# Kernel optimization log

Hardware: AMD Instinct MI355X
Metric: run time of the kernel (lower is better)

The kernel has to match this reference:

```python
import jax, jax.numpy as jnp
import numpy as np

# Vanilla tanh-RNN (num_layers=1, batch_first) followed by tanh + dropout(eval: identity) + linear.

def setup_inputs() -> dict:
    key = jax.random.key(0)
    ks = jax.random.split(key, 7)
    B, T, I, H, C = 16384, 64, 64, 100, 40
    s_ih = 1.0 / np.sqrt(H)
    return {
        "x": jax.random.normal(ks[0], (B, T * I), dtype=jnp.float32),
        "W_ih": jax.random.normal(ks[1], (H, I), dtype=jnp.float32) * s_ih,
        "W_hh": jax.random.normal(ks[2], (H, H), dtype=jnp.float32) * s_ih,
        "b_ih": jax.random.normal(ks[3], (H,), dtype=jnp.float32) * s_ih,
        "b_hh": jax.random.normal(ks[4], (H,), dtype=jnp.float32) * s_ih,
        "fc_W": jax.random.normal(ks[5], (C, H), dtype=jnp.float32) * 0.1,
        "fc_b": jax.random.normal(ks[6], (C,), dtype=jnp.float32) * 0.1,
    }


def reference(x, W_ih, W_hh, b_ih, b_hh, fc_W, fc_b):
    B = x.shape[0]
    x = x.reshape(B, 64, 64)  # [B, T, I]
    # Precompute input projections for all steps in one GEMM: [B, T, H]
    xp = jnp.einsum("bti,hi->bth", x, W_ih) + b_ih + b_hh
    h0 = jnp.zeros((B, W_hh.shape[0]), dtype=x.dtype)

    def step(h, xp_t):  # h: [B, H], xp_t: [B, H]
        h_new = jnp.tanh(xp_t + h @ W_hh.T)
        return h_new, None

    h_last, _ = jax.lax.scan(step, h0, jnp.swapaxes(xp, 0, 1))  # scan over T
    out = jnp.tanh(h_last)  # tanh on last-step output
    # dropout(p=0.2) in eval mode = identity
    return out @ fc_W.T + fc_b  # [B, 40]
```

## Files before the change

### kernel.cpp

```cpp
#include <hip/hip_runtime.h>


typedef _Float16 half8 __attribute__((ext_vector_type(8)));
typedef float float4_t __attribute__((ext_vector_type(4)));

__device__ __forceinline__ float tanh_fast(float x) {
  float e = __builtin_amdgcn_exp2f(x * 2.8853900817779268f);
  return 1.0f - 2.0f * __builtin_amdgcn_rcpf(e + 1.0f);
}

__global__ __launch_bounds__(256, 1) void rnn_fused(
    const float* __restrict__ x, const float* __restrict__ W_ih,
    const float* __restrict__ W_hh, const float* __restrict__ b_ih,
    const float* __restrict__ b_hh, const float* __restrict__ fc_W,
    const float* __restrict__ fc_b, float* __restrict__ out, int B)
{
  const int lane = threadIdx.x & 63;
  const int wave = threadIdx.x >> 6;
  const int g = lane >> 4;
  const int c = lane & 15;
  const int rowbase = (blockIdx.x * 4 + wave) * 16;

  half8 wih[2][7];
  half8 whh[4][7];
  float4_t bias[7];

  #pragma unroll
  for (int nt = 0; nt < 7; ++nt) {
    int nb = nt * 16 + 4 * g;
    float4_t bi = {0.f, 0.f, 0.f, 0.f};
    if (nb + 3 < 100) {
      float4_t a = *(const float4_t*)(b_ih + nb);
      float4_t b = *(const float4_t*)(b_hh + nb);
      bi = a + b;
    }
    bias[nt] = bi;

    int nrow = nt * 16 + c;
    bool rv = (nrow < 100);
    #pragma unroll
    for (int kb = 0; kb < 2; ++kb) {
      float4_t f0 = {0.f,0.f,0.f,0.f}, f1 = {0.f,0.f,0.f,0.f};
      if (rv) {
        const float* p = W_ih + nrow * 64 + kb * 32 + g * 8;
        f0 = *(const float4_t*)p;
        f1 = *(const float4_t*)(p + 4);
      }
      half8 h;
      #pragma unroll
      for (int j = 0; j < 4; ++j) { h[j] = (_Float16)f0[j]; h[4 + j] = (_Float16)f1[j]; }
      wih[kb][nt] = h;
    }
    #pragma unroll
    for (int kb = 0; kb < 4; ++kb) {
      int clo = kb * 32 + 4 * g;
      int chi = clo + 16;
      float4_t f0 = {0.f,0.f,0.f,0.f}, f1 = {0.f,0.f,0.f,0.f};
      if (rv && clo + 3 < 100) f0 = *(const float4_t*)(W_hh + nrow * 100 + clo);
      if (rv && chi + 3 < 100) f1 = *(const float4_t*)(W_hh + nrow * 100 + chi);
      half8 h;
      #pragma unroll
      for (int j = 0; j < 4; ++j) { h[j] = (_Float16)f0[j]; h[4 + j] = (_Float16)f1[j]; }
      whh[kb][nt] = h;
    }
  }

  const float* xrow = x + (size_t)(rowbase + c) * 4096 + g * 8;
  float4_t s0, s1, s2, s3;
  float4_t p0, p1, p2, p3;
  {
    const float* p = xrow;
    s0 = *(const float4_t*)p;        s1 = *(const float4_t*)(p + 4);
    s2 = *(const float4_t*)(p + 32); s3 = *(const float4_t*)(p + 36);
    p += 64;
    p0 = *(const float4_t*)p;        p1 = *(const float4_t*)(p + 4);
    p2 = *(const float4_t*)(p + 32); p3 = *(const float4_t*)(p + 36);
  }

  float4_t acc[7];
  half8 hfrag[4];
  #pragma unroll
  for (int kb = 0; kb < 4; ++kb) hfrag[kb] = (half8)(_Float16)0.0f;

  for (int t = 0; t < 64; ++t) {
    float4_t q0 = {0.f,0.f,0.f,0.f}, q1 = q0, q2 = q0, q3 = q0;
    if (t < 62) {
      const float* p = xrow + (t + 2) * 64;
      q0 = *(const float4_t*)p;        q1 = *(const float4_t*)(p + 4);
      q2 = *(const float4_t*)(p + 32); q3 = *(const float4_t*)(p + 36);
    }

    half8 xb0, xb1;
    #pragma unroll
    for (int j = 0; j < 4; ++j) {
      xb0[j] = (_Float16)s0[j]; xb0[4 + j] = (_Float16)s1[j];
      xb1[j] = (_Float16)s2[j]; xb1[4 + j] = (_Float16)s3[j];
    }

    #pragma unroll
    for (int nt = 0; nt < 7; ++nt) {
      acc[nt] = __builtin_amdgcn_mfma_f32_16x16x32_f16(wih[0][nt], xb0, bias[nt], 0, 0, 0);
      acc[nt] = __builtin_amdgcn_mfma_f32_16x16x32_f16(wih[1][nt], xb1, acc[nt], 0, 0, 0);
    }
    #pragma unroll
    for (int kb = 0; kb < 4; ++kb)
      #pragma unroll
      for (int nt = 0; nt < 7; ++nt)
        acc[nt] = __builtin_amdgcn_mfma_f32_16x16x32_f16(whh[kb][nt], hfrag[kb], acc[nt], 0, 0, 0);

    #pragma unroll
    for (int nt = 0; nt < 7; ++nt)
      #pragma unroll
      for (int v = 0; v < 4; ++v)
        acc[nt][v] = tanh_fast(acc[nt][v]);

    #pragma unroll
    for (int kb = 0; kb < 4; ++kb) {
      half8 h;
      #pragma unroll
      for (int v = 0; v < 4; ++v) {
        h[v] = (_Float16)acc[2 * kb][v];
        h[4 + v] = (kb < 3) ? (_Float16)acc[2 * kb + 1][v] : (_Float16)0.0f;
      }
      hfrag[kb] = h;
    }

    s0 = p0; s1 = p1; s2 = p2; s3 = p3;
    p0 = q0; p1 = q1; p2 = q2; p3 = q3;
  }

  #pragma unroll
  for (int nt = 0; nt < 7; ++nt)
    #pragma unroll
    for (int v = 0; v < 4; ++v)
      acc[nt][v] = tanh_fast(acc[nt][v]);
  #pragma unroll
  for (int kb = 0; kb < 4; ++kb) {
    half8 h;
    #pragma unroll
    for (int v = 0; v < 4; ++v) {
      h[v] = (_Float16)acc[2 * kb][v];
      h[4 + v] = (kb < 3) ? (_Float16)acc[2 * kb + 1][v] : (_Float16)0.0f;
    }
    hfrag[kb] = h;
  }

  half8 wfc[4][3];
  float4_t bfc[3];
  #pragma unroll
  for (int nt = 0; nt < 3; ++nt) {
    int nb = nt * 16 + 4 * g;
    float4_t bi = {0.f,0.f,0.f,0.f};
    if (nb + 3 < 40) bi = *(const float4_t*)(fc_b + nb);
    bfc[nt] = bi;

    int nrow = nt * 16 + c;
    bool rv = (nrow < 40);
    #pragma unroll
    for (int kb = 0; kb < 4; ++kb) {
      int clo = kb * 32 + 4 * g;
      int chi = clo + 16;
      float4_t f0 = {0.f,0.f,0.f,0.f}, f1 = {0.f,0.f,0.f,0.f};
      if (rv && clo + 3 < 100) f0 = *(const float4_t*)(fc_W + nrow * 100 + clo);
      if (rv && chi + 3 < 100) f1 = *(const float4_t*)(fc_W + nrow * 100 + chi);
      half8 h;
      #pragma unroll
      for (int j = 0; j < 4; ++j) { h[j] = (_Float16)f0[j]; h[4 + j] = (_Float16)f1[j]; }
      wfc[kb][nt] = h;
    }
  }

  float4_t oacc[3];
  #pragma unroll
  for (int nt = 0; nt < 3; ++nt) oacc[nt] = bfc[nt];
  #pragma unroll
  for (int kb = 0; kb < 4; ++kb)
    #pragma unroll
    for (int nt = 0; nt < 3; ++nt)
      oacc[nt] = __builtin_amdgcn_mfma_f32_16x16x32_f16(wfc[kb][nt], hfrag[kb], oacc[nt], 0, 0, 0);

  #pragma unroll
  for (int nt = 0; nt < 3; ++nt)
    #pragma unroll
    for (int v = 0; v < 4; ++v) {
      int n = nt * 16 + 4 * g + v;
      if (n < 40)
        out[(size_t)(rowbase + c) * 40 + n] = oacc[nt][v];
    }
}

extern "C" void kernel_launch(void* const* d_in, const int* in_sizes, int n_in,
                              void* d_out, int out_size, void* d_ws, size_t ws_size,
                              hipStream_t stream) {
  const float* x    = (const float*)d_in[0];
  const float* W_ih = (const float*)d_in[1];
  const float* W_hh = (const float*)d_in[2];
  const float* b_ih = (const float*)d_in[3];
  const float* b_hh = (const float*)d_in[4];
  const float* fc_W = (const float*)d_in[5];
  const float* fc_b = (const float*)d_in[6];
  float* outp = (float*)d_out;

  int B = in_sizes[0] / 4096;
  int grid = (B + 63) / 64;
  rnn_fused<<<grid, 256, 0, stream>>>(x, W_ih, W_hh, b_ih, b_hh, fc_W, fc_b, outp, B);
}
```

Before: 68.48 us.

## Stream x tiles into per-wave LDS ring via async global_load_lds

Replaces per-lane strided register prefetch of x with a 4-slot per-wave LDS ring filled by global_load_lds, three timesteps ahead, using coalesced row chunks with a padded layout (17-float stride). Also reorders the MFMAs so the recurrent W_hh products come first, giving the LDS reads time to land before the input-projection MFMAs. This aims at better-coalesced global loads and less register pressure, at the cost of LDS traffic and a hand-written vmcnt wait that relies on the exact count of outstanding loads.

```diff
diff --git a/kernel.cpp b/kernel.cpp
--- a/kernel.cpp
+++ b/kernel.cpp
@@ -3,6 +3,12 @@
 
 typedef _Float16 half8 __attribute__((ext_vector_type(8)));
 typedef float float4_t __attribute__((ext_vector_type(4)));
+
+#define SLOT_BYTES 5120
+#define GLOAD16(gp, lp)                                                   \
+  __builtin_amdgcn_global_load_lds(                                       \
+      (const __attribute__((address_space(1))) void*)(gp),                \
+      (__attribute__((address_space(3))) void*)(lp), 16, 0, 0)
 
 __device__ __forceinline__ float tanh_fast(float x) {
   float e = __builtin_amdgcn_exp2f(x * 2.8853900817779268f);
@@ -15,11 +21,13 @@
     const float* __restrict__ b_hh, const float* __restrict__ fc_W,
     const float* __restrict__ fc_b, float* __restrict__ out, int B)
 {
+  __shared__ char ring[4][4 * SLOT_BYTES];
   const int lane = threadIdx.x & 63;
   const int wave = threadIdx.x >> 6;
   const int g = lane >> 4;
   const int c = lane & 15;
   const int rowbase = (blockIdx.x * 4 + wave) * 16;
+  char* ring_w = &ring[wave][0];
 
   half8 wih[2][7];
   half8 whh[4][7];
@@ -65,30 +73,54 @@
     }
   }
 
-  const float* xrow = x + (size_t)(rowbase + c) * 4096 + g * 8;
-  float4_t s0, s1, s2, s3;
-  float4_t p0, p1, p2, p3;
-  {
-    const float* p = xrow;
-    s0 = *(const float4_t*)p;        s1 = *(const float4_t*)(p + 4);
-    s2 = *(const float4_t*)(p + 32); s3 = *(const float4_t*)(p + 36);
-    p += 64;
-    p0 = *(const float4_t*)p;        p1 = *(const float4_t*)(p + 4);
-    p2 = *(const float4_t*)(p + 32); p3 = *(const float4_t*)(p + 36);
-  }
+  const float* gsrc[5];
+  #pragma unroll
+  for (int j = 0; j < 5; ++j) {
+    int m = j * 64 + lane;
+    int r = (m * 3856) >> 16;
+    int c17 = m - r * 17;
+    bool valid = (r < 16) & (c17 < 16);
+    int row = rowbase + (valid ? r : 0);
+    int col = valid ? c17 * 4 : 0;
+    gsrc[j] = x + (size_t)row * 4096 + col;
+  }
+
+  #pragma unroll
+  for (int s = 0; s < 3; ++s)
+    #pragma unroll
+    for (int j = 0; j < 5; ++j)
+      GLOAD16(gsrc[j] + s * 64, ring_w + s * SLOT_BYTES + j * 1024);
 
   float4_t acc[7];
   half8 hfrag[4];
   #pragma unroll
   for (int kb = 0; kb < 4; ++kb) hfrag[kb] = (half8)(_Float16)0.0f;
 
+  const int roff = c * 272 + g * 32;
+
   for (int t = 0; t < 64; ++t) {
-    float4_t q0 = {0.f,0.f,0.f,0.f}, q1 = q0, q2 = q0, q3 = q0;
-    if (t < 62) {
-      const float* p = xrow + (t + 2) * 64;
-      q0 = *(const float4_t*)p;        q1 = *(const float4_t*)(p + 4);
-      q2 = *(const float4_t*)(p + 32); q3 = *(const float4_t*)(p + 36);
-    }
+    int tp = t + 3; if (tp > 63) tp = 63;
+    char* lb = ring_w + ((t + 3) & 3) * SLOT_BYTES;
+    #pragma unroll
+    for (int j = 0; j < 5; ++j)
+      GLOAD16(gsrc[j] + tp * 64, lb + j * 1024);
+
+    asm volatile("s_waitcnt vmcnt(15)" ::: "memory");
+
+    const char* sp = ring_w + (t & 3) * SLOT_BYTES + roff;
+    float4_t s0 = *(const float4_t*)(sp);
+    float4_t s1 = *(const float4_t*)(sp + 16);
+    float4_t s2 = *(const float4_t*)(sp + 128);
+    float4_t s3 = *(const float4_t*)(sp + 144);
+
+    #pragma unroll
+    for (int nt = 0; nt < 7; ++nt)
+      acc[nt] = __builtin_amdgcn_mfma_f32_16x16x32_f16(whh[0][nt], hfrag[0], bias[nt], 0, 0, 0);
+    #pragma unroll
+    for (int kb = 1; kb < 4; ++kb)
+      #pragma unroll
+      for (int nt = 0; nt < 7; ++nt)
+        acc[nt] = __builtin_amdgcn_mfma_f32_16x16x32_f16(whh[kb][nt], hfrag[kb], acc[nt], 0, 0, 0);
 
     half8 xb0, xb1;
     #pragma unroll
@@ -96,17 +128,11 @@
       xb0[j] = (_Float16)s0[j]; xb0[4 + j] = (_Float16)s1[j];
       xb1[j] = (_Float16)s2[j]; xb1[4 + j] = (_Float16)s3[j];
     }
-
     #pragma unroll
     for (int nt = 0; nt < 7; ++nt) {
-      acc[nt] = __builtin_amdgcn_mfma_f32_16x16x32_f16(wih[0][nt], xb0, bias[nt], 0, 0, 0);
+      acc[nt] = __builtin_amdgcn_mfma_f32_16x16x32_f16(wih[0][nt], xb0, acc[nt], 0, 0, 0);
       acc[nt] = __builtin_amdgcn_mfma_f32_16x16x32_f16(wih[1][nt], xb1, acc[nt], 0, 0, 0);
     }
-    #pragma unroll
-    for (int kb = 0; kb < 4; ++kb)
-      #pragma unroll
-      for (int nt = 0; nt < 7; ++nt)
-        acc[nt] = __builtin_amdgcn_mfma_f32_16x16x32_f16(whh[kb][nt], hfrag[kb], acc[nt], 0, 0, 0);
 
     #pragma unroll
     for (int nt = 0; nt < 7; ++nt)
@@ -124,9 +150,6 @@
       }
       hfrag[kb] = h;
     }
-
-    s0 = p0; s1 = p1; s2 = p2; s3 = p3;
-    p0 = q0; p1 = q1; p2 = q2; p3 = q3;
   }
 
   #pragma unroll
```

Result: faster. 65.51 us (-4.3%).

## Split hidden-state tiles across two waves with LDS exchange and async x prefetch ring

Applied to the files above, without the earlier changes.

Each 16-row batch tile is now processed by two waves that split the 7 hidden output tiles (4 and 3). The waves exchange their halves of the hidden state through a double-buffered LDS area, with a barrier every step. The x input is streamed into a 4-slot LDS ring using global_load_lds direct loads issued three steps ahead, replacing per-thread register prefetch. This halves the per-wave MFMA chain on the recurrent critical path and quadruples the block count, at the cost of a per-step barrier and LDS round trip.

```diff
diff --git a/kernel.cpp b/kernel.cpp
--- a/kernel.cpp
+++ b/kernel.cpp
@@ -3,30 +3,44 @@
 
 typedef _Float16 half8 __attribute__((ext_vector_type(8)));
 typedef float float4_t __attribute__((ext_vector_type(4)));
+
+#define SLOT_BYTES 6144
+#define RING_BYTES (4 * SLOT_BYTES)
+#define HX_BYTES 4096
+#define GLOAD16(gp, lp)                                                   \
+  __builtin_amdgcn_global_load_lds(                                       \
+      (const __attribute__((address_space(1))) void*)(gp),                \
+      (__attribute__((address_space(3))) void*)(lp), 16, 0, 0)
 
 __device__ __forceinline__ float tanh_fast(float x) {
   float e = __builtin_amdgcn_exp2f(x * 2.8853900817779268f);
   return 1.0f - 2.0f * __builtin_amdgcn_rcpf(e + 1.0f);
 }
 
-__global__ __launch_bounds__(256, 1) void rnn_fused(
+template <int NTBASE, int NTN, int FCB, int FCN>
+__device__ __forceinline__ void run_tile(
     const float* __restrict__ x, const float* __restrict__ W_ih,
     const float* __restrict__ W_hh, const float* __restrict__ b_ih,
     const float* __restrict__ b_hh, const float* __restrict__ fc_W,
-    const float* __restrict__ fc_b, float* __restrict__ out, int B)
+    const float* __restrict__ fc_b, float* __restrict__ out,
+    int rowbase, int lane, int wave, char* ldsp)
 {
-  const int lane = threadIdx.x & 63;
-  const int wave = threadIdx.x >> 6;
   const int g = lane >> 4;
   const int c = lane & 15;
-  const int rowbase = (blockIdx.x * 4 + wave) * 16;
-
-  half8 wih[2][7];
-  half8 whh[4][7];
-  float4_t bias[7];
-
-  #pragma unroll
-  for (int nt = 0; nt < 7; ++nt) {
+  constexpr int K0 = NTBASE / 2;
+  constexpr int FKB = K0 ^ 2;
+
+  const unsigned ring_base =
+      (unsigned)(uintptr_t)(__attribute__((address_space(3))) char*)ldsp;
+  const unsigned hx_base = ring_base + RING_BYTES;
+
+  half8 wih[2][NTN];
+  half8 whh[4][NTN];
+  float4_t bias[NTN];
+
+  #pragma unroll
+  for (int nl = 0; nl < NTN; ++nl) {
+    int nt = NTBASE + nl;
     int nb = nt * 16 + 4 * g;
     float4_t bi = {0.f, 0.f, 0.f, 0.f};
     if (nb + 3 < 100) {
@@ -34,7 +48,7 @@
       float4_t b = *(const float4_t*)(b_hh + nb);
       bi = a + b;
     }
-    bias[nt] = bi;
+    bias[nl] = bi;
 
     int nrow = nt * 16 + c;
     bool rv = (nrow < 100);
@@ -49,7 +63,7 @@
       half8 h;
       #pragma unroll
       for (int j = 0; j < 4; ++j) { h[j] = (_Float16)f0[j]; h[4 + j] = (_Float16)f1[j]; }
-      wih[kb][nt] = h;
+      wih[kb][nl] = h;
     }
     #pragma unroll
     for (int kb = 0; kb < 4; ++kb) {
@@ -61,33 +75,74 @@
       half8 h;
       #pragma unroll
       for (int j = 0; j < 4; ++j) { h[j] = (_Float16)f0[j]; h[4 + j] = (_Float16)f1[j]; }
-      whh[kb][nt] = h;
-    }
-  }
-
-  const float* xrow = x + (size_t)(rowbase + c) * 4096 + g * 8;
-  float4_t s0, s1, s2, s3;
-  float4_t p0, p1, p2, p3;
+      whh[kb][nl] = h;
+    }
+  }
+
+  const float* gsrc[3];
+  #pragma unroll
+  for (int j = 0; j < 3; ++j) {
+    int m = j * 128 + wave * 64 + lane;
+    int r = (m * 3856) >> 16;
+    int c17 = m - r * 17;
+    bool valid = (r < 16) & (c17 < 16);
+    int row = rowbase + (valid ? r : 0);
+    int col = valid ? c17 * 4 : 0;
+    gsrc[j] = x + (size_t)row * 4096 + col;
+  }
+
+  #pragma unroll
+  for (int s = 0; s < 3; ++s) {
+    char* lb = ldsp + s * SLOT_BYTES + wave * 1024;
+    GLOAD16(gsrc[0] + s * 64, lb);
+    GLOAD16(gsrc[1] + s * 64, lb + 2048);
+    GLOAD16(gsrc[2] + s * 64, lb + 4096);
+  }
+
+  half8 own0 = (half8)(_Float16)0.0f;
+  half8 own1 = (half8)(_Float16)0.0f;
   {
-    const float* p = xrow;
-    s0 = *(const float4_t*)p;        s1 = *(const float4_t*)(p + 4);
-    s2 = *(const float4_t*)(p + 32); s3 = *(const float4_t*)(p + 36);
-    p += 64;
-    p0 = *(const float4_t*)p;        p1 = *(const float4_t*)(p + 4);
-    p2 = *(const float4_t*)(p + 32); p3 = *(const float4_t*)(p + 36);
-  }
-
-  float4_t acc[7];
-  half8 hfrag[4];
-  #pragma unroll
-  for (int kb = 0; kb < 4; ++kb) hfrag[kb] = (half8)(_Float16)0.0f;
+    unsigned wa = hx_base + K0 * 1024 + c * 64 + g * 16;
+    asm volatile(
+        "ds_write_b128 %0, %1 offset:0\n\t"
+        "ds_write_b128 %0, %2 offset:1024"
+        :: "v"(wa), "v"(__builtin_bit_cast(float4_t, own0)),
+           "v"(__builtin_bit_cast(float4_t, own1)));
+  }
+  asm volatile("s_waitcnt vmcnt(6) lgkmcnt(0)\n\ts_barrier" ::: "memory");
+
+  float4_t acc[4];
 
   for (int t = 0; t < 64; ++t) {
-    float4_t q0 = {0.f,0.f,0.f,0.f}, q1 = q0, q2 = q0, q3 = q0;
-    if (t < 62) {
-      const float* p = xrow + (t + 2) * 64;
-      q0 = *(const float4_t*)p;        q1 = *(const float4_t*)(p + 4);
-      q2 = *(const float4_t*)(p + 32); q3 = *(const float4_t*)(p + 36);
+    unsigned ha = hx_base + (t & 1) * HX_BYTES + FKB * 1024 + c * 64 + g * 16;
+    unsigned xa = ring_base + (t & 3) * SLOT_BYTES + c * 272 + g * 32;
+    float4_t fh0, fh1, s0, s1, s2, s3;
+    asm volatile(
+        "ds_read_b128 %0, %6 offset:0\n\t"
+        "ds_read_b128 %1, %6 offset:1024\n\t"
+        "ds_read_b128 %2, %7 offset:0\n\t"
+        "ds_read_b128 %3, %7 offset:16\n\t"
+        "ds_read_b128 %4, %7 offset:128\n\t"
+        "ds_read_b128 %5, %7 offset:144"
+        : "=&v"(fh0), "=&v"(fh1), "=&v"(s0), "=&v"(s1), "=&v"(s2), "=&v"(s3)
+        : "v"(ha), "v"(xa));
+
+    #pragma unroll
+    for (int nl = 0; nl < NTN; ++nl) {
+      acc[nl] = __builtin_amdgcn_mfma_f32_16x16x32_f16(whh[K0][nl], own0, bias[nl], 0, 0, 0);
+      acc[nl] = __builtin_amdgcn_mfma_f32_16x16x32_f16(whh[K0 + 1][nl], own1, acc[nl], 0, 0, 0);
+    }
+
+    asm volatile("s_waitcnt lgkmcnt(0)"
+                 : "+v"(fh0), "+v"(fh1), "+v"(s0), "+v"(s1), "+v"(s2), "+v"(s3));
+    __builtin_amdgcn_sched_barrier(0);
+
+    half8 fr0 = __builtin_bit_cast(half8, fh0);
+    half8 fr1 = __builtin_bit_cast(half8, fh1);
+    #pragma unroll
+    for (int nl = 0; nl < NTN; ++nl) {
+      acc[nl] = __builtin_amdgcn_mfma_f32_16x16x32_f16(whh[FKB][nl], fr0, acc[nl], 0, 0, 0);
+      acc[nl] = __builtin_amdgcn_mfma_f32_16x16x32_f16(whh[FKB + 1][nl], fr1, acc[nl], 0, 0, 0);
     }
 
     half8 xb0, xb1;
@@ -96,65 +151,89 @@
       xb0[j] = (_Float16)s0[j]; xb0[4 + j] = (_Float16)s1[j];
       xb1[j] = (_Float16)s2[j]; xb1[4 + j] = (_Float16)s3[j];
     }
-
-    #pragma unroll
-    for (int nt = 0; nt < 7; ++nt) {
-      acc[nt] = __builtin_amdgcn_mfma_f32_16x16x32_f16(wih[0][nt], xb0, bias[nt], 0, 0, 0);
-      acc[nt] = __builtin_amdgcn_mfma_f32_16x16x32_f16(wih[1][nt], xb1, acc[nt], 0, 0, 0);
-    }
-    #pragma unroll
-    for (int kb = 0; kb < 4; ++kb)
-      #pragma unroll
-      for (int nt = 0; nt < 7; ++nt)
-        acc[nt] = __builtin_amdgcn_mfma_f32_16x16x32_f16(whh[kb][nt], hfrag[kb], acc[nt], 0, 0, 0);
-
-    #pragma unroll
-    for (int nt = 0; nt < 7; ++nt)
+    #pragma unroll
+    for (int nl = 0; nl < NTN; ++nl) {
+      acc[nl] = __builtin_amdgcn_mfma_f32_16x16x32_f16(wih[0][nl], xb0, acc[nl], 0, 0, 0);
+      acc[nl] = __builtin_amdgcn_mfma_f32_16x16x32_f16(wih[1][nl], xb1, acc[nl], 0, 0, 0);
+    }
+
+    #pragma unroll
+    for (int nl = 0; nl < NTN; ++nl)
       #pragma unroll
       for (int v = 0; v < 4; ++v)
-        acc[nt][v] = tanh_fast(acc[nt][v]);
-
-    #pragma unroll
-    for (int kb = 0; kb < 4; ++kb) {
-      half8 h;
-      #pragma unroll
-      for (int v = 0; v < 4; ++v) {
-        h[v] = (_Float16)acc[2 * kb][v];
-        h[4 + v] = (kb < 3) ? (_Float16)acc[2 * kb + 1][v] : (_Float16)0.0f;
-      }
-      hfrag[kb] = h;
-    }
-
-    s0 = p0; s1 = p1; s2 = p2; s3 = p3;
-    p0 = q0; p1 = q1; p2 = q2; p3 = q3;
-  }
-
-  #pragma unroll
-  for (int nt = 0; nt < 7; ++nt)
+        acc[nl][v] = tanh_fast(acc[nl][v]);
+
+    #pragma unroll
+    for (int v = 0; v < 4; ++v) {
+      own0[v]     = (_Float16)acc[0][v];
+      own0[4 + v] = (NTN > 1) ? (_Float16)acc[1][v] : (_Float16)0.0f;
+      own1[v]     = (NTN > 2) ? (_Float16)acc[2][v] : (_Float16)0.0f;
+      own1[4 + v] = (NTN > 3) ? (_Float16)acc[3][v] : (_Float16)0.0f;
+    }
+
+    unsigned wa = hx_base + ((t + 1) & 1) * HX_BYTES + K0 * 1024 + c * 64 + g * 16;
+    asm volatile(
+        "ds_write_b128 %0, %1 offset:0\n\t"
+        "ds_write_b128 %0, %2 offset:1024"
+        :: "v"(wa), "v"(__builtin_bit_cast(float4_t, own0)),
+           "v"(__builtin_bit_cast(float4_t, own1)));
+
+    int tp = t + 3; if (tp > 63) tp = 63;
+    char* lb = ldsp + ((t + 3) & 3) * SLOT_BYTES + wave * 1024;
+    GLOAD16(gsrc[0] + tp * 64, lb);
+    GLOAD16(gsrc[1] + tp * 64, lb + 2048);
+    GLOAD16(gsrc[2] + tp * 64, lb + 4096);
+
+    asm volatile("s_waitcnt vmcnt(6) lgkmcnt(0)\n\ts_barrier" ::: "memory");
+  }
+
+  #pragma unroll
+  for (int nl = 0; nl < NTN; ++nl)
     #pragma unroll
     for (int v = 0; v < 4; ++v)
-      acc[nt][v] = tanh_fast(acc[nt][v]);
-  #pragma unroll
-  for (int kb = 0; kb < 4; ++kb) {
-    half8 h;
-    #pragma unroll
-    for (int v = 0; v < 4; ++v) {
-      h[v] = (_Float16)acc[2 * kb][v];
-      h[4 + v] = (kb < 3) ? (_Float16)acc[2 * kb + 1][v] : (_Float16)0.0f;
-    }
-    hfrag[kb] = h;
-  }
-
-  half8 wfc[4][3];
-  float4_t bfc[3];
-  #pragma unroll
-  for (int nt = 0; nt < 3; ++nt) {
-    int nb = nt * 16 + 4 * g;
+      acc[nl][v] = tanh_fast(acc[nl][v]);
+  #pragma unroll
+  for (int v = 0; v < 4; ++v) {
+    own0[v]     = (_Float16)acc[0][v];
+    own0[4 + v] = (NTN > 1) ? (_Float16)acc[1][v] : (_Float16)0.0f;
+    own1[v]     = (NTN > 2) ? (_Float16)acc[2][v] : (_Float16)0.0f;
+    own1[4 + v] = (NTN > 3) ? (_Float16)acc[3][v] : (_Float16)0.0f;
+  }
+  {
+    unsigned wa = hx_base + HX_BYTES + K0 * 1024 + c * 64 + g * 16;
+    asm volatile(
+        "ds_write_b128 %0, %1 offset:0\n\t"
+        "ds_write_b128 %0, %2 offset:1024"
+        :: "v"(wa), "v"(__builtin_bit_cast(float4_t, own0)),
+           "v"(__builtin_bit_cast(float4_t, own1)));
+  }
+  asm volatile("s_waitcnt lgkmcnt(0)\n\ts_barrier" ::: "memory");
+
+  float4_t fz0, fz1;
+  {
+    unsigned ra = hx_base + HX_BYTES + FKB * 1024 + c * 64 + g * 16;
+    asm volatile(
+        "ds_read_b128 %0, %2 offset:0\n\t"
+        "ds_read_b128 %1, %2 offset:1024\n\t"
+        "s_waitcnt lgkmcnt(0)"
+        : "=&v"(fz0), "=&v"(fz1) : "v"(ra));
+  }
+  half8 zf[4];
+  zf[K0] = own0; zf[K0 + 1] = own1;
+  zf[FKB] = __builtin_bit_cast(half8, fz0);
+  zf[FKB + 1] = __builtin_bit_cast(half8, fz1);
+
+  half8 wfc[4][FCN];
+  float4_t bfc[FCN];
+  #pragma unroll
+  for (int ft = 0; ft < FCN; ++ft) {
+    int fct = FCB + ft;
+    int nb = fct * 16 + 4 * g;
     float4_t bi = {0.f,0.f,0.f,0.f};
     if (nb + 3 < 40) bi = *(const float4_t*)(fc_b + nb);
-    bfc[nt] = bi;
-
-    int nrow = nt * 16 + c;
+    bfc[ft] = bi;
+
+    int nrow = fct * 16 + c;
     bool rv = (nrow < 40);
     #pragma unroll
     for (int kb = 0; kb < 4; ++kb) {
@@ -166,27 +245,48 @@
       half8 h;
       #pragma unroll
       for (int j = 0; j < 4; ++j) { h[j] = (_Float16)f0[j]; h[4 + j] = (_Float16)f1[j]; }
-      wfc[kb][nt] = h;
-    }
-  }
-
-  float4_t oacc[3];
-  #pragma unroll
-  for (int nt = 0; nt < 3; ++nt) oacc[nt] = bfc[nt];
+      wfc[kb][ft] = h;
+    }
+  }
+
+  float4_t oacc[FCN];
+  #pragma unroll
+  for (int ft = 0; ft < FCN; ++ft) oacc[ft] = bfc[ft];
   #pragma unroll
   for (int kb = 0; kb < 4; ++kb)
     #pragma unroll
-    for (int nt = 0; nt < 3; ++nt)
-      oacc[nt] = __builtin_amdgcn_mfma_f32_16x16x32_f16(wfc[kb][nt], hfrag[kb], oacc[nt], 0, 0, 0);
-
-  #pragma unroll
-  for (int nt = 0; nt < 3; ++nt)
+    for (int ft = 0; ft < FCN; ++ft)
+      oacc[ft] = __builtin_amdgcn_mfma_f32_16x16x32_f16(wfc[kb][ft], zf[kb], oacc[ft], 0, 0, 0);
+
+  #pragma unroll
+  for (int ft = 0; ft < FCN; ++ft)
     #pragma unroll
     for (int v = 0; v < 4; ++v) {
-      int n = nt * 16 + 4 * g + v;
+      int n = (FCB + ft) * 16 + 4 * g + v;
       if (n < 40)
-        out[(size_t)(rowbase + c) * 40 + n] = oacc[nt][v];
-    }
+        out[(size_t)(rowbase + c) * 40 + n] = oacc[ft][v];
+    }
+}
+
+__global__ __launch_bounds__(128, 2) void rnn_fused(
+    const float* __restrict__ x, const float* __restrict__ W_ih,
+    const float* __restrict__ W_hh, const float* __restrict__ b_ih,
+    const float* __restrict__ b_hh, const float* __restrict__ fc_W,
+    const float* __restrict__ fc_b, float* __restrict__ out, int B)
+{
+  __shared__ char lds[RING_BYTES + 2 * HX_BYTES];
+  const int lane = threadIdx.x & 63;
+  const int wave = threadIdx.x >> 6;
+  const int role = (wave ^ (blockIdx.x & 1)) & 1;
+  const int rowbase = blockIdx.x * 16;
+  if (rowbase >= B) return;
+
+  if (role == 0)
+    run_tile<0, 4, 0, 2>(x, W_ih, W_hh, b_ih, b_hh, fc_W, fc_b, out,
+                         rowbase, lane, wave, lds);
+  else
+    run_tile<4, 3, 2, 1>(x, W_ih, W_hh, b_ih, b_hh, fc_W, fc_b, out,
+                         rowbase, lane, wave, lds);
 }
 
 extern "C" void kernel_launch(void* const* d_in, const int* in_sizes, int n_in,
@@ -202,6 +302,6 @@
   float* outp = (float*)d_out;
 
   int B = in_sizes[0] / 4096;
-  int grid = (B + 63) / 64;
-  rnn_fused<<<grid, 256, 0, stream>>>(x, W_ih, W_hh, b_ih, b_hh, fc_W, fc_b, outp, B);
+  int grid = (B + 15) / 16;
+  rnn_fused<<<grid, 128, 0, stream>>>(x, W_ih, W_hh, b_ih, b_hh, fc_W, fc_b, outp, B);
 }
```

Result: no change. 67.81 us (-1.0%).
